# Kernel optimization log

Measured on AMD Instinct MI355X. Metric: run time of the kernel, lower is better.

Reference implementation:

```python
import jax, jax.numpy as jnp
import numpy as np

NUM_EMB = 1024
EMB_DIM = 32


def setup_inputs() -> dict:
    key = jax.random.key(0)
    k1, k2 = jax.random.split(key)
    z = jax.random.normal(k1, (32, EMB_DIM, 64, 64), dtype=jnp.float32)
    # nn.Embedding weight init: uniform(-1/num_embeddings, 1/num_embeddings)
    emb_weight = jax.random.uniform(
        k2, (NUM_EMB, EMB_DIM), dtype=jnp.float32,
        minval=-1.0 / NUM_EMB, maxval=1.0 / NUM_EMB)
    return {"z": z, "emb_weight": emb_weight}


def reference(z, emb_weight):
    # z: [B, C, H, W] -> [B, H, W, C]
    z_p = jnp.transpose(z, (0, 2, 3, 1))
    B, H, W, C = z_p.shape
    z_flat = z_p.reshape(-1, C)  # [N, C]
    # squared distances via expansion: ||z||^2 + ||e||^2 - 2 z.e  -> [N, K]
    d = (jnp.sum(z_flat * z_flat, axis=1, keepdims=True)
         + jnp.sum(emb_weight * emb_weight, axis=1)
         - 2.0 * jnp.matmul(z_flat, emb_weight.T))
    idx = jnp.argmin(d, axis=1)  # [N]
    z_q = emb_weight[idx].reshape(B, H, W, C)
    # straight-through estimator (applied in BHWC, then back to BCHW)
    z_q = z_p + jax.lax.stop_gradient(z_q - z_p)
    z_q = jnp.transpose(z_q, (0, 3, 1, 2))  # [B, C, H, W]
    return z_q, idx
```

## Files before the change

kernel.cpp:

```cpp
#include <hip/hip_runtime.h>


#define NUM_EMB 1024
#define EMB_DIM 32
#define HW      4096
#define BATCH   32
#define N_TOT   (BATCH * HW)
#define NSPLIT  4
#define CODES_PER (NUM_EMB / NSPLIT)
#define MARGIN  1.0e-4f
#define CHUNK   256

#define OFF_BQ    0u
#define OFF_EH    4096u
#define WS_NEED   69632u
#define WS_NEED_R7 (4096u + 4u * 131072u * 8u)

using f16x8 = __attribute__((ext_vector_type(8))) _Float16;
using f32x4 = __attribute__((ext_vector_type(4))) float;

#define REPEAT32(M) \
    M(0)  M(1)  M(2)  M(3)  M(4)  M(5)  M(6)  M(7)  \
    M(8)  M(9)  M(10) M(11) M(12) M(13) M(14) M(15) \
    M(16) M(17) M(18) M(19) M(20) M(21) M(22) M(23) \
    M(24) M(25) M(26) M(27) M(28) M(29) M(30) M(31)

__device__ __forceinline__ float pairwise_sq32(const float* __restrict__ e) {
    float r0 = __fmul_rn(e[0], e[0]), r1 = __fmul_rn(e[1], e[1]);
    float r2 = __fmul_rn(e[2], e[2]), r3 = __fmul_rn(e[3], e[3]);
    float r4 = __fmul_rn(e[4], e[4]), r5 = __fmul_rn(e[5], e[5]);
    float r6 = __fmul_rn(e[6], e[6]), r7 = __fmul_rn(e[7], e[7]);
#pragma unroll
    for (int i = 8; i < 32; i += 8) {
        r0 = __fadd_rn(r0, __fmul_rn(e[i + 0], e[i + 0]));
        r1 = __fadd_rn(r1, __fmul_rn(e[i + 1], e[i + 1]));
        r2 = __fadd_rn(r2, __fmul_rn(e[i + 2], e[i + 2]));
        r3 = __fadd_rn(r3, __fmul_rn(e[i + 3], e[i + 3]));
        r4 = __fadd_rn(r4, __fmul_rn(e[i + 4], e[i + 4]));
        r5 = __fadd_rn(r5, __fmul_rn(e[i + 5], e[i + 5]));
        r6 = __fadd_rn(r6, __fmul_rn(e[i + 6], e[i + 6]));
        r7 = __fadd_rn(r7, __fmul_rn(e[i + 7], e[i + 7]));
    }
    return __fadd_rn(__fadd_rn(__fadd_rn(r0, r1), __fadd_rn(r2, r3)),
                     __fadd_rn(__fadd_rn(r4, r5), __fadd_rn(r6, r7)));
}

__device__ __forceinline__ void store_row16(unsigned short* dst,
                                            const unsigned short* v) {
    unsigned w[16];
#pragma unroll
    for (int i = 0; i < 16; ++i)
        w[i] = (unsigned)v[2 * i] | ((unsigned)v[2 * i + 1] << 16);
    uint4* d4 = (uint4*)dst;
    d4[0] = make_uint4(w[0], w[1], w[2], w[3]);
    d4[1] = make_uint4(w[4], w[5], w[6], w[7]);
    d4[2] = make_uint4(w[8], w[9], w[10], w[11]);
    d4[3] = make_uint4(w[12], w[13], w[14], w[15]);
}

__global__ __launch_bounds__(256) void vq_prep_e(
        const float* __restrict__ emb, float* __restrict__ bq,
        unsigned short* __restrict__ eh) {
    const int g = blockIdx.x * 256 + threadIdx.x;
    if (g >= NUM_EMB) return;
    const float* e = emb + g * EMB_DIM;
    bq[g] = pairwise_sq32(e);
    unsigned short h[32];
#pragma unroll
    for (int c = 0; c < 32; ++c) {
        _Float16 hv = (_Float16)(-2.0f * e[c]);
        h[c] = __builtin_bit_cast(unsigned short, hv);
    }
    store_row16(eh + (size_t)g * 32, h);
}

#define LOADZ(c) float z##c = zp[(size_t)(c) * HW];
#define Z_SQ_A()                                                              \
    float r0 = __fmul_rn(z0, z0), r1 = __fmul_rn(z1, z1);                     \
    float r2 = __fmul_rn(z2, z2), r3 = __fmul_rn(z3, z3);                     \
    float r4 = __fmul_rn(z4, z4), r5 = __fmul_rn(z5, z5);                     \
    float r6 = __fmul_rn(z6, z6), r7 = __fmul_rn(z7, z7);                     \
    r0 = __fadd_rn(r0, __fmul_rn(z8,  z8));  r0 = __fadd_rn(r0, __fmul_rn(z16, z16)); \
    r0 = __fadd_rn(r0, __fmul_rn(z24, z24));                                  \
    r1 = __fadd_rn(r1, __fmul_rn(z9,  z9));  r1 = __fadd_rn(r1, __fmul_rn(z17, z17)); \
    r1 = __fadd_rn(r1, __fmul_rn(z25, z25));                                  \
    r2 = __fadd_rn(r2, __fmul_rn(z10, z10)); r2 = __fadd_rn(r2, __fmul_rn(z18, z18)); \
    r2 = __fadd_rn(r2, __fmul_rn(z26, z26));                                  \
    r3 = __fadd_rn(r3, __fmul_rn(z11, z11)); r3 = __fadd_rn(r3, __fmul_rn(z19, z19)); \
    r3 = __fadd_rn(r3, __fmul_rn(z27, z27));                                  \
    r4 = __fadd_rn(r4, __fmul_rn(z12, z12)); r4 = __fadd_rn(r4, __fmul_rn(z20, z20)); \
    r4 = __fadd_rn(r4, __fmul_rn(z28, z28));                                  \
    r5 = __fadd_rn(r5, __fmul_rn(z13, z13)); r5 = __fadd_rn(r5, __fmul_rn(z21, z21)); \
    r5 = __fadd_rn(r5, __fmul_rn(z29, z29));                                  \
    r6 = __fadd_rn(r6, __fmul_rn(z14, z14)); r6 = __fadd_rn(r6, __fmul_rn(z22, z22)); \
    r6 = __fadd_rn(r6, __fmul_rn(z30, z30));                                  \
    r7 = __fadd_rn(r7, __fmul_rn(z15, z15)); r7 = __fadd_rn(r7, __fmul_rn(z23, z23)); \
    r7 = __fadd_rn(r7, __fmul_rn(z31, z31));                                  \
    const float a = __fadd_rn(                                                \
        __fadd_rn(__fadd_rn(r0, r1), __fadd_rn(r2, r3)),                      \
        __fadd_rn(__fadd_rn(r4, r5), __fadd_rn(r6, r7)));

#define FMA1(k) m = __fmaf_rn(z##k, e[(k)], m);
#define EXACT_KEY(jv)                                                         \
    {                                                                         \
        const float* e = emb + (size_t)(jv) * EMB_DIM;                        \
        float m = 0.0f;                                                       \
        REPEAT32(FMA1)                                                        \
        float d = __fsub_rn(__fadd_rn(a, bq[(jv)]), __fmul_rn(2.0f, m));      \
        unsigned u = __float_as_uint(d);                                      \
        u = (u & 0x80000000u) ? ~u : (u | 0x80000000u);                       \
        unsigned long long kk =                                               \
            ((unsigned long long)u << 32) | (unsigned)(jv);                   \
        if (kk < bestk) bestk = kk;                                           \
    }

__global__ __launch_bounds__(256, 4) void vq_filter(
        const float* __restrict__ z, const float* __restrict__ emb,
        const unsigned short* __restrict__ eh,
        const float* __restrict__ bq,
        float* __restrict__ out_zq, float* __restrict__ out_idx) {
    __shared__ __align__(16) char smem[17408];
    _Float16* seh = (_Float16*)smem;
    float*    sbq = (float*)(smem + 16384);
    int* scand  = (int*)smem;
    int* sdest  = (int*)(smem + 2048);
    int* sBlist = (int*)(smem + 2560);
    unsigned long long* bs =
        (unsigned long long*)(smem + 3072);
    __shared__ int swt[2];

    const int tid  = threadIdx.x;
    const int lane = tid & 63;
    const int wv   = tid >> 6;
    const int cloc = lane & 15, quad = lane >> 4;
    const int qbase = blockIdx.x * 128 + wv * 32;

    f16x8 az[2];
#pragma unroll
    for (int t = 0; t < 2; ++t) {
        const int q  = qbase + t * 16 + cloc;
        const int b  = q >> 12;
        const int hw = q & 4095;
        const float* zb = z + ((size_t)b * EMB_DIM + quad * 8) * HW + hw;
#pragma unroll
        for (int k = 0; k < 8; ++k)
            az[t][k] = (_Float16)zb[(size_t)k * HW];
    }

    float m1[2][4], m2[2][4];
#pragma unroll
    for (int t = 0; t < 2; ++t)
#pragma unroll
        for (int r = 0; r < 4; ++r) { m1[t][r] = 3.4e38f; m2[t][r] = 3.4e38f; }

    const unsigned km = 0xFFFFFFC0u;

    for (int ch = 0; ch < 4; ++ch) {
        if (ch) __syncthreads();
        {
            const uint4* src = (const uint4*)(eh + (size_t)ch * CHUNK * 32);
            uint4* dst = (uint4*)seh;
#pragma unroll
            for (int i = 0; i < 4; ++i) dst[i * 256 + tid] = src[i * 256 + tid];
            sbq[tid] = bq[ch * CHUNK + tid];
        }
        __syncthreads();

        float c1[2][4], c2[2][4];
#pragma unroll
        for (int t = 0; t < 2; ++t)
#pragma unroll
            for (int r = 0; r < 4; ++r) { c1[t][r] = 3.4e38f; c2[t][r] = 3.4e38f; }

#pragma unroll
        for (int jt = 0; jt < 16; ++jt) {
            const int row = jt * 16 + cloc;
            f16x8 ef = *(const f16x8*)(seh + row * 32 + quad * 8);
            const float bqv = sbq[row];
#pragma unroll
            for (int t = 0; t < 2; ++t) {
                f32x4 acc = {bqv, bqv, bqv, bqv};
                acc = __builtin_amdgcn_mfma_f32_16x16x32_f16(az[t], ef, acc, 0, 0, 0);
#pragma unroll
                for (int r = 0; r < 4; ++r) {
                    const float kv = __uint_as_float(
                        (__float_as_uint(acc[r]) & km) | (unsigned)jt);
                    c2[t][r] = __builtin_amdgcn_fmed3f(kv, c1[t][r], c2[t][r]);
                    c1[t][r] = fminf(c1[t][r], kv);
                }
            }
        }

        const unsigned chb = (unsigned)ch << 4;
#pragma unroll
        for (int t = 0; t < 2; ++t)
#pragma unroll
            for (int r = 0; r < 4; ++r) {
                const float a1 = __uint_as_float(__float_as_uint(c1[t][r]) | chb);
                const float a2 = __uint_as_float(__float_as_uint(c2[t][r]) | chb);
                m2[t][r] = fminf(fmaxf(m1[t][r], a1), fminf(m2[t][r], a2));
                m1[t][r] = fminf(m1[t][r], a1);
            }
    }
    __syncthreads();

    float g[2][4];
#pragma unroll
    for (int t = 0; t < 2; ++t)
#pragma unroll
        for (int r = 0; r < 4; ++r) g[t][r] = m1[t][r];
#pragma unroll
    for (int off = 1; off < 16; off <<= 1)
#pragma unroll
        for (int t = 0; t < 2; ++t)
#pragma unroll
            for (int r = 0; r < 4; ++r)
                g[t][r] = fminf(g[t][r], __shfl_xor(g[t][r], off, 64));

#pragma unroll
    for (int t = 0; t < 2; ++t)
#pragma unroll
        for (int r = 0; r < 4; ++r) {
            const float thr = g[t][r] + MARGIN;
            const int   ql  = wv * 32 + t * 16 + quad * 4 + r;
            const bool  f1  = m1[t][r] <= thr;
            const bool  f2  = m2[t][r] <= thr;
            const unsigned long long b1 = __ballot(f1);
            const unsigned long long b2 = __ballot(f2);
            const unsigned mk1 = (unsigned)(b1 >> (quad * 16)) & 0xFFFFu;
            const unsigned mk2 = (unsigned)(b2 >> (quad * 16)) & 0xFFFFu;
            const int pc  = __popc(mk1);
            const int ldr = __ffs(mk1) - 1;
            if (mk2 | (unsigned)(pc > 4)) {
                if (cloc == ldr) sdest[ql] = 5;
            } else {
                if (f1)
                    scand[(ql << 2) + __popc(mk1 & ((1u << cloc) - 1u))] =
                        (int)(__float_as_uint(m1[t][r]) & 63u) * 16 + cloc;
                if (cloc == ldr) sdest[ql] = pc;
            }
        }
    __syncthreads();

    int d = 0, pre = 0;
    if (tid < 128) {
        d = sdest[tid];
        const unsigned long long mB = __ballot(d == 5);
        pre = (int)__popcll(mB & ((1ull << lane) - 1ull));
        if (lane == 0) swt[tid >> 6] = (int)__popcll(mB);
    }
    __syncthreads();
    int myidx = 0;
    if (tid < 128) {
        if (d == 5) {
            sBlist[((tid >> 6) ? swt[0] : 0) + pre] = tid;
        } else if (d == 1) {
            myidx = scand[tid << 2];
        } else {
            const int n  = blockIdx.x * 128 + tid;
            const int bb = n >> 12;
            const int hh = n & 4095;
            const float* zp = z + (size_t)bb * EMB_DIM * HW + hh;
            REPEAT32(LOADZ)
            Z_SQ_A()
            unsigned long long bestk = ~0ull;
            for (int k = 0; k < d; ++k) {
                const int jv = scand[(tid << 2) + k];
                EXACT_KEY(jv)
            }
            myidx = (int)(unsigned)(bestk & 0xffffffffu);
        }
    }
    __syncthreads();

    if (tid < 128 && d != 5) {
        const int n    = blockIdx.x * 128 + tid;
        out_idx[n] = (float)myidx;
        const int bb = n >> 12;
        const int hh = n & 4095;
        const float4* er = (const float4*)(emb + (size_t)myidx * EMB_DIM);
        float* op = out_zq + (size_t)bb * EMB_DIM * HW + hh;
#pragma unroll
        for (int c4 = 0; c4 < 8; ++c4) {
            float4 v = er[c4];
            op[(size_t)(c4 * 4 + 0) * HW] = v.x;
            op[(size_t)(c4 * 4 + 1) * HW] = v.y;
            op[(size_t)(c4 * 4 + 2) * HW] = v.z;
            op[(size_t)(c4 * 4 + 3) * HW] = v.w;
        }
    }

    const int nB = swt[0] + swt[1];
    for (int ib = 0; ib < nB; ++ib) {
        const int ql = sBlist[ib];
        const int n  = blockIdx.x * 128 + ql;
        const int bb = n >> 12;
        const int hh = n & 4095;
        const float* zp = z + (size_t)bb * EMB_DIM * HW + hh;
        REPEAT32(LOADZ)
        Z_SQ_A()
        unsigned long long bestk = ~0ull;
#pragma unroll
        for (int k = 0; k < 4; ++k) { const int jv = tid * 4 + k; EXACT_KEY(jv) }
        bs[tid] = bestk;
        __syncthreads();
        for (int off = 128; off > 0; off >>= 1) {
            if (tid < off && bs[tid + off] < bs[tid]) bs[tid] = bs[tid + off];
            __syncthreads();
        }
        const int fb = (int)(unsigned)(bs[0] & 0xffffffffu);
        if (tid == 0) out_idx[n] = (float)fb;
        if (tid < EMB_DIM)
            out_zq[(size_t)bb * EMB_DIM * HW + (size_t)tid * HW + hh] =
                emb[(size_t)fb * EMB_DIM + tid];
        __syncthreads();
    }
}

#define SCAN_GROUP4(j)                                                        \
    {                                                                         \
        const float* e = emb + (size_t)(j) * EMB_DIM;                         \
        const float bq0 = bq[(j) + 0], bq1 = bq[(j) + 1];                     \
        const float bq2 = bq[(j) + 2], bq3 = bq[(j) + 3];                     \
        float m0 = 0.0f, m1 = 0.0f, m2 = 0.0f, m3 = 0.0f;                     \
        REPEAT32(FMA_K)                                                       \
        float d0 = __fsub_rn(__fadd_rn(a, bq0), __fmul_rn(2.0f, m0));         \
        float d1 = __fsub_rn(__fadd_rn(a, bq1), __fmul_rn(2.0f, m1));         \
        float d2 = __fsub_rn(__fadd_rn(a, bq2), __fmul_rn(2.0f, m2));         \
        float d3 = __fsub_rn(__fadd_rn(a, bq3), __fmul_rn(2.0f, m3));         \
        if (d0 < best) { best = d0; bidx = (j) + 0; }                         \
        if (d1 < best) { best = d1; bidx = (j) + 1; }                         \
        if (d2 < best) { best = d2; bidx = (j) + 2; }                         \
        if (d3 < best) { best = d3; bidx = (j) + 3; }                         \
    }
#define FMA_K(k) \
        m0 = __fmaf_rn(z##k, e[0 * EMB_DIM + (k)], m0); \
        m1 = __fmaf_rn(z##k, e[1 * EMB_DIM + (k)], m1); \
        m2 = __fmaf_rn(z##k, e[2 * EMB_DIM + (k)], m2); \
        m3 = __fmaf_rn(z##k, e[3 * EMB_DIM + (k)], m3);

__global__ __launch_bounds__(256) void vq_sqnorm_kernel(
        const float* __restrict__ emb, float* __restrict__ bq) {
    int j = blockIdx.x * 256 + threadIdx.x;
    if (j < NUM_EMB) bq[j] = pairwise_sq32(emb + j * EMB_DIM);
}

__global__ __launch_bounds__(128, 4) void vq_partial_kernel(
        const float* __restrict__ z, const float* __restrict__ emb,
        const float* __restrict__ bq, unsigned long long* __restrict__ pk) {
    const int n  = blockIdx.x * 128 + threadIdx.x;
    const int b  = n >> 12;
    const int hw = n & 4095;
    const float* zp = z + (size_t)b * EMB_DIM * HW + hw;
    REPEAT32(LOADZ)
    Z_SQ_A()
    const int j0 = blockIdx.y * CODES_PER;
    float best = 3.4e38f;
    int   bidx = j0;
    for (int j = j0; j < j0 + CODES_PER; j += 4) SCAN_GROUP4(j)
    pk[(size_t)blockIdx.y * N_TOT + n] =
        ((unsigned long long)__float_as_uint(best) << 32) | (unsigned)bidx;
}

__global__ __launch_bounds__(256, 2) void vq_main_kernel(
        const float* __restrict__ z, const float* __restrict__ emb,
        const float* __restrict__ bq, float* __restrict__ out_zq,
        float* __restrict__ out_idx) {
    const int n  = blockIdx.x * 256 + threadIdx.x;
    const int b  = n >> 12;
    const int hw = n & 4095;
    const float* zp = z + (size_t)b * EMB_DIM * HW + hw;
    REPEAT32(LOADZ)
    Z_SQ_A()
    float best = 3.4e38f;
    int   bidx = 0;
    for (int j = 0; j < NUM_EMB; j += 4) SCAN_GROUP4(j)
    out_idx[n] = (float)bidx;
    const float* eb = emb + (size_t)bidx * EMB_DIM;
    float* op = out_zq + (size_t)b * EMB_DIM * HW + hw;
#pragma unroll
    for (int cc = 0; cc < EMB_DIM; ++cc) op[(size_t)cc * HW] = eb[cc];
}

__global__ __launch_bounds__(256) void vq_combine_kernel(
        const float* __restrict__ emb,
        const unsigned long long* __restrict__ pk,
        float* __restrict__ out_zq, float* __restrict__ out_idx) {
    const int n = blockIdx.x * 256 + threadIdx.x;
    unsigned long long m = pk[n];
#pragma unroll
    for (int y = 1; y < NSPLIT; ++y) {
        unsigned long long v = pk[(size_t)y * N_TOT + n];
        if (v < m) m = v;
    }
    const int bidx = (int)(unsigned)(m & 0xffffffffu);
    out_idx[n] = (float)bidx;
    const int b  = n >> 12;
    const int hw = n & 4095;
    const float* eb = emb + (size_t)bidx * EMB_DIM;
    float* op = out_zq + (size_t)b * EMB_DIM * HW + hw;
#pragma unroll
    for (int cc = 0; cc < EMB_DIM; ++cc) op[(size_t)cc * HW] = eb[cc];
}

extern "C" void kernel_launch(void* const* d_in, const int* in_sizes, int n_in,
                              void* d_out, int out_size, void* d_ws,
                              size_t ws_size, hipStream_t stream) {
    const float* z   = (const float*)d_in[0];
    const float* emb = (const float*)d_in[1];
    char* ws = (char*)d_ws;
    float* out0 = (float*)d_out;
    float* out1 = out0 + (size_t)BATCH * EMB_DIM * HW;

    if (ws_size >= WS_NEED) {
        float*          bq = (float*)(ws + OFF_BQ);
        unsigned short* eh = (unsigned short*)(ws + OFF_EH);

        vq_prep_e<<<4, 256, 0, stream>>>(emb, bq, eh);
        vq_filter<<<N_TOT / 128, 256, 0, stream>>>(z, emb, eh, bq,
                                                   out0, out1);
    } else if (ws_size >= WS_NEED_R7) {
        float* bq = (float*)ws;
        unsigned long long* pk = (unsigned long long*)(ws + 4096);
        vq_sqnorm_kernel<<<NUM_EMB / 256, 256, 0, stream>>>(emb, bq);
        vq_partial_kernel<<<dim3(N_TOT / 128, NSPLIT), 128, 0, stream>>>(
            z, emb, bq, pk);
        vq_combine_kernel<<<N_TOT / 256, 256, 0, stream>>>(emb, pk, out0, out1);
    } else {
        float* bq = (float*)ws;
        vq_sqnorm_kernel<<<NUM_EMB / 256, 256, 0, stream>>>(emb, bq);
        vq_main_kernel<<<N_TOT / 256, 256, 0, stream>>>(z, emb, bq, out0, out1);
    }
}
```

Baseline: 131.7 us.

## Double-buffer codebook chunks in LDS with register prefetch

Codebook chunks are now staged through a two-buffer LDS ring. The next chunk's fp16 embeddings and biases are prefetched into registers while the MFMA scan runs on the current chunk, then written to the other buffer. This removes one barrier per chunk and hides global load latency behind compute. In exchange, LDS per block doubles to about 34 KB and register pressure rises, which could lower occupancy under launch_bounds(256,4).

Result: slower. 383.9 us (+191.5%).

```diff
diff --git a/kernel.cpp b/kernel.cpp
--- a/kernel.cpp
+++ b/kernel.cpp
@@ -119,15 +119,14 @@
         const unsigned short* __restrict__ eh,
         const float* __restrict__ bq,
         float* __restrict__ out_zq, float* __restrict__ out_idx) {
-    __shared__ __align__(16) char smem[17408];
-    _Float16* seh = (_Float16*)smem;
-    float*    sbq = (float*)(smem + 16384);
+    __shared__ __align__(16) char smem[34816];
+    __shared__ int swt[2];
+    __shared__ int snB;
     int* scand  = (int*)smem;
     int* sdest  = (int*)(smem + 2048);
     int* sBlist = (int*)(smem + 2560);
     unsigned long long* bs =
         (unsigned long long*)(smem + 3072);
-    __shared__ int swt[2];
 
     const int tid  = threadIdx.x;
     const int lane = tid & 63;
@@ -135,6 +134,13 @@
     const int cloc = lane & 15, quad = lane >> 4;
     const int qbase = blockIdx.x * 128 + wv * 32;
 
+    const uint4* esrc = (const uint4*)eh;
+    uint4 sreg0 = esrc[tid];
+    uint4 sreg1 = esrc[256 + tid];
+    uint4 sreg2 = esrc[512 + tid];
+    uint4 sreg3 = esrc[768 + tid];
+    float breg  = bq[tid];
+
     f16x8 az[2];
 #pragma unroll
     for (int t = 0; t < 2; ++t) {
@@ -147,6 +153,16 @@
             az[t][k] = (_Float16)zb[(size_t)k * HW];
     }
 
+    {
+        uint4* dst = (uint4*)smem;
+        dst[tid]       = sreg0;
+        dst[256 + tid] = sreg1;
+        dst[512 + tid] = sreg2;
+        dst[768 + tid] = sreg3;
+        ((float*)(smem + 32768))[tid] = breg;
+    }
+    __syncthreads();
+
     float m1[2][4], m2[2][4];
 #pragma unroll
     for (int t = 0; t < 2; ++t)
@@ -154,18 +170,23 @@
         for (int r = 0; r < 4; ++r) { m1[t][r] = 3.4e38f; m2[t][r] = 3.4e38f; }
 
     const unsigned km = 0xFFFFFFC0u;
-
+    const int fbase = cloc * 64 + quad * 16;
+
+#pragma unroll
     for (int ch = 0; ch < 4; ++ch) {
-        if (ch) __syncthreads();
-        {
-            const uint4* src = (const uint4*)(eh + (size_t)ch * CHUNK * 32);
-            uint4* dst = (uint4*)seh;
-#pragma unroll
-            for (int i = 0; i < 4; ++i) dst[i * 256 + tid] = src[i * 256 + tid];
-            sbq[tid] = bq[ch * CHUNK + tid];
-        }
-        __syncthreads();
-
+        const int cur = ch & 1;
+
+        if (ch < 3) {
+            const int cb = (ch + 1) * 1024;
+            sreg0 = esrc[cb + tid];
+            sreg1 = esrc[cb + 256 + tid];
+            sreg2 = esrc[cb + 512 + tid];
+            sreg3 = esrc[cb + 768 + tid];
+            breg  = bq[(ch + 1) * 256 + tid];
+        }
+
+        const char*  bufe = smem + cur * 16384;
+        const float* sb   = (const float*)(smem + 32768 + cur * 1024);
         float c1[2][4], c2[2][4];
 #pragma unroll
         for (int t = 0; t < 2; ++t)
@@ -174,9 +195,8 @@
 
 #pragma unroll
         for (int jt = 0; jt < 16; ++jt) {
-            const int row = jt * 16 + cloc;
-            f16x8 ef = *(const f16x8*)(seh + row * 32 + quad * 8);
-            const float bqv = sbq[row];
+            f16x8 ef = *(const f16x8*)(bufe + fbase + jt * 1024);
+            const float bqv = sb[jt * 16 + cloc];
 #pragma unroll
             for (int t = 0; t < 2; ++t) {
                 f32x4 acc = {bqv, bqv, bqv, bqv};
@@ -191,6 +211,16 @@
             }
         }
 
+        if (ch < 3) {
+            uint4* dst = (uint4*)(smem + (cur ^ 1) * 16384);
+            dst[tid]       = sreg0;
+            dst[256 + tid] = sreg1;
+            dst[512 + tid] = sreg2;
+            dst[768 + tid] = sreg3;
+            ((float*)(smem + 32768 + (cur ^ 1) * 1024))[tid] = breg;
+        }
+        __syncthreads();
+
         const unsigned chb = (unsigned)ch << 4;
 #pragma unroll
         for (int t = 0; t < 2; ++t)
@@ -202,7 +232,6 @@
                 m1[t][r] = fminf(m1[t][r], a1);
             }
     }
-    __syncthreads();
 
     float g[2][4];
 #pragma unroll
@@ -242,7 +271,7 @@
         }
     __syncthreads();
 
-    int d = 0, pre = 0;
+    int d = 0, pre = 0, myidx = 0;
     if (tid < 128) {
         d = sdest[tid];
         const unsigned long long mB = __ballot(d == 5);
@@ -250,7 +279,7 @@
         if (lane == 0) swt[tid >> 6] = (int)__popcll(mB);
     }
     __syncthreads();
-    int myidx = 0;
+    if (tid == 0) snB = swt[0] + swt[1];
     if (tid < 128) {
         if (d == 5) {
             sBlist[((tid >> 6) ? swt[0] : 0) + pre] = tid;
@@ -274,7 +303,7 @@
     __syncthreads();
 
     if (tid < 128 && d != 5) {
-        const int n    = blockIdx.x * 128 + tid;
+        const int n = blockIdx.x * 128 + tid;
         out_idx[n] = (float)myidx;
         const int bb = n >> 12;
         const int hh = n & 4095;
@@ -290,7 +319,7 @@
         }
     }
 
-    const int nB = swt[0] + swt[1];
+    const int nB = snB;
     for (int ib = 0; ib < nB; ++ib) {
         const int ql = sBlist[ib];
         const int n  = blockIdx.x * 128 + ql;
```

## Read fp16 codebook directly from global memory instead of staging through LDS

Applied to the files above, without the earlier changes.

Drops the four-chunk LDS staging of the fp16 codebook and its bias, along with the syncthreads around each chunk. Each lane now loads its MFMA B fragment and bias straight from global memory (expected to be cache-resident) across a single 64-tile loop. The per-chunk top-2 merge is gone, so tile indices 0..63 fill the low 6 key bits directly. This frees LDS and barriers, which may raise occupancy, at the cost of more global/L2 load latency inside the MFMA loop.

Result: slower. 138.9 us (+5.5%).

```diff
diff --git a/kernel.cpp b/kernel.cpp
--- a/kernel.cpp
+++ b/kernel.cpp
@@ -9,7 +9,6 @@
 #define NSPLIT  4
 #define CODES_PER (NUM_EMB / NSPLIT)
 #define MARGIN  1.0e-4f
-#define CHUNK   256
 
 #define OFF_BQ    0u
 #define OFF_EH    4096u
@@ -119,15 +118,12 @@
         const unsigned short* __restrict__ eh,
         const float* __restrict__ bq,
         float* __restrict__ out_zq, float* __restrict__ out_idx) {
-    __shared__ __align__(16) char smem[17408];
-    _Float16* seh = (_Float16*)smem;
-    float*    sbq = (float*)(smem + 16384);
-    int* scand  = (int*)smem;
-    int* sdest  = (int*)(smem + 2048);
-    int* sBlist = (int*)(smem + 2560);
-    unsigned long long* bs =
-        (unsigned long long*)(smem + 3072);
+    __shared__ int scand[512];
+    __shared__ int sdest[128];
+    __shared__ int sBlist[128];
+    __shared__ unsigned long long bs[256];
     __shared__ int swt[2];
+    __shared__ int snB;
 
     const int tid  = threadIdx.x;
     const int lane = tid & 63;
@@ -154,55 +150,26 @@
         for (int r = 0; r < 4; ++r) { m1[t][r] = 3.4e38f; m2[t][r] = 3.4e38f; }
 
     const unsigned km = 0xFFFFFFC0u;
-
-    for (int ch = 0; ch < 4; ++ch) {
-        if (ch) __syncthreads();
-        {
-            const uint4* src = (const uint4*)(eh + (size_t)ch * CHUNK * 32);
-            uint4* dst = (uint4*)seh;
-#pragma unroll
-            for (int i = 0; i < 4; ++i) dst[i * 256 + tid] = src[i * 256 + tid];
-            sbq[tid] = bq[ch * CHUNK + tid];
-        }
-        __syncthreads();
-
-        float c1[2][4], c2[2][4];
-#pragma unroll
-        for (int t = 0; t < 2; ++t)
-#pragma unroll
-            for (int r = 0; r < 4; ++r) { c1[t][r] = 3.4e38f; c2[t][r] = 3.4e38f; }
-
-#pragma unroll
-        for (int jt = 0; jt < 16; ++jt) {
-            const int row = jt * 16 + cloc;
-            f16x8 ef = *(const f16x8*)(seh + row * 32 + quad * 8);
-            const float bqv = sbq[row];
-#pragma unroll
-            for (int t = 0; t < 2; ++t) {
-                f32x4 acc = {bqv, bqv, bqv, bqv};
-                acc = __builtin_amdgcn_mfma_f32_16x16x32_f16(az[t], ef, acc, 0, 0, 0);
-#pragma unroll
-                for (int r = 0; r < 4; ++r) {
-                    const float kv = __uint_as_float(
-                        (__float_as_uint(acc[r]) & km) | (unsigned)jt);
-                    c2[t][r] = __builtin_amdgcn_fmed3f(kv, c1[t][r], c2[t][r]);
-                    c1[t][r] = fminf(c1[t][r], kv);
-                }
+    const char* efp = (const char*)eh + cloc * 64 + quad * 16;
+    const float* bqp = bq + cloc;
+
+#pragma unroll 8
+    for (int jt = 0; jt < 64; ++jt) {
+        const f16x8 ef  = *(const f16x8*)(efp + jt * 1024);
+        const float bqv = bqp[jt * 16];
+#pragma unroll
+        for (int t = 0; t < 2; ++t) {
+            f32x4 acc = {bqv, bqv, bqv, bqv};
+            acc = __builtin_amdgcn_mfma_f32_16x16x32_f16(az[t], ef, acc, 0, 0, 0);
+#pragma unroll
+            for (int r = 0; r < 4; ++r) {
+                const float kv = __uint_as_float(
+                    (__float_as_uint(acc[r]) & km) | (unsigned)jt);
+                m2[t][r] = __builtin_amdgcn_fmed3f(kv, m1[t][r], m2[t][r]);
+                m1[t][r] = fminf(m1[t][r], kv);
             }
         }
-
-        const unsigned chb = (unsigned)ch << 4;
-#pragma unroll
-        for (int t = 0; t < 2; ++t)
-#pragma unroll
-            for (int r = 0; r < 4; ++r) {
-                const float a1 = __uint_as_float(__float_as_uint(c1[t][r]) | chb);
-                const float a2 = __uint_as_float(__float_as_uint(c2[t][r]) | chb);
-                m2[t][r] = fminf(fmaxf(m1[t][r], a1), fminf(m2[t][r], a2));
-                m1[t][r] = fminf(m1[t][r], a1);
-            }
-    }
-    __syncthreads();
+    }
 
     float g[2][4];
 #pragma unroll
@@ -242,7 +209,7 @@
         }
     __syncthreads();
 
-    int d = 0, pre = 0;
+    int d = 0, pre = 0, myidx = 0;
     if (tid < 128) {
         d = sdest[tid];
         const unsigned long long mB = __ballot(d == 5);
@@ -250,7 +217,7 @@
         if (lane == 0) swt[tid >> 6] = (int)__popcll(mB);
     }
     __syncthreads();
-    int myidx = 0;
+    if (tid == 0) snB = swt[0] + swt[1];
     if (tid < 128) {
         if (d == 5) {
             sBlist[((tid >> 6) ? swt[0] : 0) + pre] = tid;
@@ -274,7 +241,7 @@
     __syncthreads();
 
     if (tid < 128 && d != 5) {
-        const int n    = blockIdx.x * 128 + tid;
+        const int n = blockIdx.x * 128 + tid;
         out_idx[n] = (float)myidx;
         const int bb = n >> 12;
         const int hh = n & 4095;
@@ -290,7 +257,7 @@
         }
     }
 
-    const int nB = swt[0] + swt[1];
+    const int nB = snB;
     for (int ib = 0; ib < nB; ++ib) {
         const int ql = sBlist[ib];
         const int n  = blockIdx.x * 128 + ql;
```
